# Kernel tuning notes

Hardware: AMD Instinct MI355X
Metric: run time of the kernel (lower is better)

The kernel has to match this reference:

```python
import jax, jax.numpy as jnp
import numpy as np

N = 40000          # nodes
E = 640000         # edges (avg degree 16)
D_MODEL = 128
H = 8              # num_heads
DH = 16            # d_head
DFF = 512
CLAMP = 5.0
EPS = 1e-5


def setup_inputs() -> dict:
    key = jax.random.key(0)
    ks = jax.random.split(key, 10)
    s = 0.08  # weight init scale
    return {
        "feat": jax.random.normal(ks[0], (N, D_MODEL), dtype=jnp.float32),
        "src": jax.random.randint(ks[1], (E,), 0, N, dtype=jnp.int32),
        "dst": jax.random.randint(ks[2], (E,), 0, N, dtype=jnp.int32),
        "Wq": jax.random.normal(ks[3], (H * DH, D_MODEL), dtype=jnp.float32) * s,
        "Wk": jax.random.normal(ks[4], (H * DH, D_MODEL), dtype=jnp.float32) * s,
        "Wv": jax.random.normal(ks[5], (H * DH, D_MODEL), dtype=jnp.float32) * s,
        "Wo": jax.random.normal(ks[6], (D_MODEL, H * DH), dtype=jnp.float32) * s,
        "ln1_g": jnp.ones((D_MODEL,), jnp.float32),
        "ln1_b": jnp.zeros((D_MODEL,), jnp.float32),
        "W1": jax.random.normal(ks[7], (DFF, D_MODEL), dtype=jnp.float32) * s,
        "b1": jnp.zeros((DFF,), jnp.float32),
        "W2": jax.random.normal(ks[8], (D_MODEL, DFF), dtype=jnp.float32) * s,
        "b2": jnp.zeros((D_MODEL,), jnp.float32),
        "ln2_g": jnp.ones((D_MODEL,), jnp.float32),
        "ln2_b": jnp.zeros((D_MODEL,), jnp.float32),
    }


def _layer_norm(x, g, b):
    mu = jnp.mean(x, axis=-1, keepdims=True)
    var = jnp.mean(jnp.square(x - mu), axis=-1, keepdims=True)
    return (x - mu) * jax.lax.rsqrt(var + EPS) * g + b


def reference(feat, src, dst, Wq, Wk, Wv, Wo, ln1_g, ln1_b, W1, b1, W2, b2, ln2_g, ln2_b):
    n = feat.shape[0]
    # Node-level projections (equivalent to DGL's per-edge Linear on gathered feats)
    q = (feat @ Wq.T).reshape(n, H, DH)
    k = (feat @ Wk.T).reshape(n, H, DH)
    v = (feat @ Wv.T).reshape(n, H, DH)

    # Per-edge multi-head attention logits: q[dst] . k[src] / sqrt(d_head), clamped
    u = jnp.sum(q[dst] * k[src], axis=-1) / np.sqrt(DH)   # [E, H]
    u = jnp.clip(u, -CLAMP, CLAMP)

    # Ragged edge-softmax over incoming edges of each dst node
    m = jax.ops.segment_max(u, dst, num_segments=n)        # [N, H]
    e = jnp.exp(u - m[dst])                                # [E, H]
    denom = jax.ops.segment_sum(e, dst, num_segments=n)    # [N, H]
    a = e / denom[dst]                                     # [E, H]

    # Weighted V scatter-reduce back to dst nodes
    av = (a[:, :, None] * v[src]).reshape(-1, H * DH)      # [E, H*DH]
    sum_av = jax.ops.segment_sum(av, dst, num_segments=n)  # [N, H*DH]
    uh = sum_av @ Wo.T                                     # [N, d_model]

    h1 = _layer_norm(feat + uh, ln1_g, ln1_b)
    ffn = jax.nn.relu(h1 @ W1.T + b1) @ W2.T + b2
    return _layer_norm(h1 + ffn, ln2_g, ln2_b)
```

## Files before the change

### kernel.cpp

```cpp
#include <hip/hip_runtime.h>

#define DM 128
#define DFF 512
#define CLAMP_V 5.0f
#define LN_EPS 1e-5f

typedef __attribute__((ext_vector_type(8))) short bf16x8;
typedef __attribute__((ext_vector_type(4))) float f32x4;
typedef __attribute__((ext_vector_type(2))) float f32x2;

__device__ __forceinline__ float b2f(ushort u) {
  union { uint u; float f; } x; x.u = ((uint)u) << 16; return x.f;
}
__device__ __forceinline__ ushort f2b(float f) {
  union { float f; uint u; } x; x.f = f;
  uint r = x.u + 0x7FFFu + ((x.u >> 16) & 1u);
  return (ushort)(r >> 16);
}
__device__ __forceinline__ f32x2 upk2(uint w) {
  union { uint u; float f; } a, b;
  a.u = w << 16; b.u = w & 0xFFFF0000u;
  f32x2 r; r[0] = a.f; r[1] = b.f; return r;
}

__global__ void k_prep(const float* __restrict__ feat,
                       const float* __restrict__ wq, const float* __restrict__ wk,
                       const float* __restrict__ wv, const float* __restrict__ wo,
                       const float* __restrict__ w1, const float* __restrict__ w2,
                       ushort* __restrict__ feat_bf, ushort* __restrict__ wbf,
                       const int* __restrict__ dst, int* __restrict__ deg,
                       int nf4, int castBlocks, int E) {
  if ((int)blockIdx.x >= castBlocks) {
    int e = ((int)blockIdx.x - castBlocks) * 256 + threadIdx.x;
    if (e < E) atomicAdd(&deg[dst[e]], 1);
    return;
  }
  int i = blockIdx.x * 256 + threadIdx.x;
  if (i < nf4) {
    float4 v = *reinterpret_cast<const float4*>(feat + i * 4);
    ushort4 o; o.x = f2b(v.x); o.y = f2b(v.y); o.z = f2b(v.z); o.w = f2b(v.w);
    *reinterpret_cast<ushort4*>(feat_bf + i * 4) = o;
    return;
  }
  int i4 = (i - nf4) * 4;
  if (i4 >= 196608) return;
  const float* s; int o;
  if      (i4 < 16384)  { s = wq; o = i4; }
  else if (i4 < 32768)  { s = wk; o = i4 - 16384; }
  else if (i4 < 49152)  { s = wv; o = i4 - 32768; }
  else if (i4 < 65536)  { s = wo; o = i4 - 49152; }
  else if (i4 < 131072) { s = w1; o = i4 - 65536; }
  else                  { s = w2; o = i4 - 131072; }
  float4 v = *reinterpret_cast<const float4*>(s + o);
  ushort4 u; u.x = f2b(v.x); u.y = f2b(v.y); u.z = f2b(v.z); u.w = f2b(v.w);
  *reinterpret_cast<ushort4*>(wbf + i4) = u;
}

#define SC_EPB 1024

__global__ __launch_bounds__(256) void k_scan(const int* __restrict__ deg,
                                              int* __restrict__ off,
                                              int* __restrict__ cur,
                                              int n, int E) {
  __shared__ int sh[256];
  __shared__ int wsum[4];
  const int t = threadIdx.x;
  const int bstart = blockIdx.x * SC_EPB;

  int gs = 0;
  for (int base = t * 4; base < bstart; base += SC_EPB) {
    int4 v = *reinterpret_cast<const int4*>(deg + base);
    gs += v.x + v.y + v.z + v.w;
  }
  #pragma unroll
  for (int m = 1; m < 64; m <<= 1) gs += __shfl_xor(gs, m);
  if ((t & 63) == 0) wsum[t >> 6] = gs;
  __syncthreads();
  int gadd = wsum[0] + wsum[1] + wsum[2] + wsum[3];
  __syncthreads();

  int base = bstart + t * 4;
  int4 v = {0, 0, 0, 0};
  if (base + 3 < n) {
    v = *reinterpret_cast<const int4*>(deg + base);
  } else {
    if (base     < n) v.x = deg[base];
    if (base + 1 < n) v.y = deg[base + 1];
    if (base + 2 < n) v.z = deg[base + 2];
    if (base + 3 < n) v.w = deg[base + 3];
  }
  int s = v.x + v.y + v.z + v.w;
  sh[t] = s;
  __syncthreads();
  #pragma unroll
  for (int d = 1; d < 256; d <<= 1) {
    int x = 0;
    if (t >= d) x = sh[t - d];
    __syncthreads();
    sh[t] += x;
    __syncthreads();
  }
  int ex = sh[t] - s + gadd;
  if (base + 3 < n) {
    int4 o; o.x = ex; o.y = ex + v.x; o.z = ex + v.x + v.y; o.w = ex + v.x + v.y + v.z;
    *reinterpret_cast<int4*>(off + base) = o;
    int4 z = {0, 0, 0, 0};
    *reinterpret_cast<int4*>(cur + base) = z;
  } else {
    if (base     < n) { off[base]     = ex;                    cur[base]     = 0; }
    if (base + 1 < n) { off[base + 1] = ex + v.x;              cur[base + 1] = 0; }
    if (base + 2 < n) { off[base + 2] = ex + v.x + v.y;        cur[base + 2] = 0; }
    if (base + 3 < n) { off[base + 3] = ex + v.x + v.y + v.z;  cur[base + 3] = 0; }
  }
  if (blockIdx.x == 0 && t == 0) off[n] = E;
}

__global__ __launch_bounds__(512, 2) void k_sqkv(
    const ushort* __restrict__ A, const ushort* __restrict__ W,
    ushort* __restrict__ Cb, ushort* __restrict__ Cb2, int M,
    const int* __restrict__ src, const int* __restrict__ dst,
    const int* __restrict__ off, int* __restrict__ cur,
    int* __restrict__ csr, int E, int qkvB)
{
  __shared__ ushort As[128 * 128];
  __shared__ ushort Bs[128 * 128];

  if ((int)blockIdx.x >= qkvB) {
    int e = ((int)blockIdx.x - qkvB) * 512 + threadIdx.x;
    if (e < E) {
      int d = dst[e];
      int p = off[d] + atomicAdd(&cur[d], 1);
      csr[p] = src[e];
    }
    return;
  }

  const int tid = threadIdx.x;
  const int wv = tid >> 6, ln = tid & 63;
  const int bnb = blockIdx.x % 3;
  const int mbase = (blockIdx.x / 3) * 128;
  const int wrow = (wv >> 2) * 64, wcol = (wv & 3) * 32;
  const int o_base = tid * 16;

  #pragma unroll
  for (int is = 0; is < 4; ++is) {
    int o = is * 8192 + o_base;
    int row = o >> 8;
    int c = ((o >> 4) & 15) ^ (row & 15);
    int gr = min(mbase + row, M - 1);
    const ushort* sA = A + (size_t)gr * 128 + c * 8;
    __builtin_amdgcn_global_load_lds(
        (const __attribute__((address_space(1))) void*)sA,
        (__attribute__((address_space(3))) void*)((char*)As + is * 8192 + wv * 1024),
        16, 0, 0);
    const ushort* sB = W + (size_t)(bnb * 128 + row) * 128 + c * 8;
    __builtin_amdgcn_global_load_lds(
        (const __attribute__((address_space(1))) void*)sB,
        (__attribute__((address_space(3))) void*)((char*)Bs + is * 8192 + wv * 1024),
        16, 0, 0);
  }
  __syncthreads();

  f32x4 acc[4][2] = {};
  const char* AsB = (const char*)As;
  const char* BsB = (const char*)Bs;
  #pragma unroll
  for (int kk = 0; kk < 4; ++kk) {
    bf16x8 af[4], bfr[2];
    #pragma unroll
    for (int m = 0; m < 4; ++m) {
      int r = wrow + m * 16 + (ln & 15);
      int c = kk * 4 + (ln >> 4);
      af[m] = *reinterpret_cast<const bf16x8*>(AsB + r * 256 + ((c ^ (r & 15)) << 4));
    }
    #pragma unroll
    for (int n = 0; n < 2; ++n) {
      int r = wcol + n * 16 + (ln & 15);
      int c = kk * 4 + (ln >> 4);
      bfr[n] = *reinterpret_cast<const bf16x8*>(BsB + r * 256 + ((c ^ (r & 15)) << 4));
    }
    #pragma unroll
    for (int m = 0; m < 4; ++m)
      #pragma unroll
      for (int n = 0; n < 2; ++n)
        acc[m][n] = __builtin_amdgcn_mfma_f32_16x16x32_bf16(af[m], bfr[n], acc[m][n], 0, 0, 0);
  }

  #pragma unroll
  for (int m = 0; m < 4; ++m) {
    int gr0 = mbase + wrow + m * 16 + (ln >> 4) * 4;
    #pragma unroll
    for (int n = 0; n < 2; ++n) {
      int gcl = wcol + n * 16 + (ln & 15);
      #pragma unroll
      for (int r = 0; r < 4; ++r) {
        int gr = gr0 + r;
        if (gr >= M) continue;
        float v = acc[m][n][r];
        if (bnb == 0) Cb[(size_t)gr * 128 + gcl] = f2b(v);
        else          Cb2[(size_t)gr * 256 + (bnb - 1) * 128 + gcl] = f2b(v);
      }
    }
  }
}

template<int FLAGS, bool OUTF, bool OUTB>
__global__ __launch_bounds__(512, 2) void k_mmT(
    const ushort* __restrict__ A, const ushort* __restrict__ W,
    const float* __restrict__ res,
    const float* __restrict__ lng, const float* __restrict__ lnbv,
    float* __restrict__ Cf, ushort* __restrict__ Cb, int M)
{
  __shared__ ushort As[128 * 128];
  __shared__ ushort Bs[128 * 128];
  __shared__ float lnred[1024];

  const int tid = threadIdx.x;
  const int wv = tid >> 6, ln = tid & 63;
  const int mbase = blockIdx.y * 128;
  const int wrow = (wv >> 2) * 64, wcol = (wv & 3) * 32;
  const int o_base = tid * 16;

  #pragma unroll
  for (int is = 0; is < 4; ++is) {
    int o = is * 8192 + o_base;
    int row = o >> 8;
    int c = ((o >> 4) & 15) ^ (row & 15);
    int gr = min(mbase + row, M - 1);
    const ushort* sA = A + (size_t)gr * 128 + c * 8;
    __builtin_amdgcn_global_load_lds(
        (const __attribute__((address_space(1))) void*)sA,
        (__attribute__((address_space(3))) void*)((char*)As + is * 8192 + wv * 1024),
        16, 0, 0);
    const ushort* sB = W + (size_t)row * 128 + c * 8;
    __builtin_amdgcn_global_load_lds(
        (const __attribute__((address_space(1))) void*)sB,
        (__attribute__((address_space(3))) void*)((char*)Bs + is * 8192 + wv * 1024),
        16, 0, 0);
  }
  __syncthreads();

  f32x4 acc[4][2] = {};
  const char* AsB = (const char*)As;
  const char* BsB = (const char*)Bs;
  #pragma unroll
  for (int kk = 0; kk < 4; ++kk) {
    bf16x8 af[4], bfr[2];
    #pragma unroll
    for (int m = 0; m < 4; ++m) {
      int r = wrow + m * 16 + (ln & 15);
      int c = kk * 4 + (ln >> 4);
      af[m] = *reinterpret_cast<const bf16x8*>(AsB + r * 256 + ((c ^ (r & 15)) << 4));
    }
    #pragma unroll
    for (int n = 0; n < 2; ++n) {
      int r = wcol + n * 16 + (ln & 15);
      int c = kk * 4 + (ln >> 4);
      bfr[n] = *reinterpret_cast<const bf16x8*>(BsB + r * 256 + ((c ^ (r & 15)) << 4));
    }
    #pragma unroll
    for (int m = 0; m < 4; ++m)
      #pragma unroll
      for (int n = 0; n < 2; ++n)
        acc[m][n] = __builtin_amdgcn_mfma_f32_16x16x32_bf16(af[m], bfr[n], acc[m][n], 0, 0, 0);
  }

  #pragma unroll
  for (int m = 0; m < 4; ++m)
    #pragma unroll
    for (int n = 0; n < 2; ++n) {
      int gc = wcol + n * 16 + (ln & 15);
      #pragma unroll
      for (int r = 0; r < 4; ++r) {
        int gr = mbase + wrow + m * 16 + (ln >> 4) * 4 + r;
        float v = acc[m][n][r];
        if (FLAGS & 4) v += res[(size_t)min(gr, M - 1) * 128 + gc];
        acc[m][n][r] = v;
      }
    }
  #pragma unroll
  for (int m = 0; m < 4; ++m)
    #pragma unroll
    for (int r = 0; r < 4; ++r) {
      float sm = acc[m][0][r] + acc[m][1][r];
      float sq = acc[m][0][r] * acc[m][0][r] + acc[m][1][r] * acc[m][1][r];
      #pragma unroll
      for (int msk = 1; msk <= 8; msk <<= 1) {
        sm += __shfl_xor(sm, msk);
        sq += __shfl_xor(sq, msk);
      }
      if ((ln & 15) == 0) {
        int row = wrow + m * 16 + (ln >> 4) * 4 + r;
        lnred[row * 8 + (wv & 3) * 2]     = sm;
        lnred[row * 8 + (wv & 3) * 2 + 1] = sq;
      }
    }
  __syncthreads();
  #pragma unroll
  for (int m = 0; m < 4; ++m)
    #pragma unroll
    for (int r = 0; r < 4; ++r) {
      int row = wrow + m * 16 + (ln >> 4) * 4 + r;
      int gr = mbase + row;
      float sm = lnred[row * 8] + lnred[row * 8 + 2] + lnred[row * 8 + 4] + lnred[row * 8 + 6];
      float sq = lnred[row * 8 + 1] + lnred[row * 8 + 3] + lnred[row * 8 + 5] + lnred[row * 8 + 7];
      float mu = sm * (1.f / 128.f);
      float var = fmaxf(sq * (1.f / 128.f) - mu * mu, 0.f);
      float rstd = rsqrtf(var + LN_EPS);
      if (gr < M) {
        #pragma unroll
        for (int n = 0; n < 2; ++n) {
          int gc = wcol + n * 16 + (ln & 15);
          float y = (acc[m][n][r] - mu) * rstd * lng[gc] + lnbv[gc];
          if (OUTF) Cf[(size_t)gr * 128 + gc] = y;
          if (OUTB) Cb[(size_t)gr * 128 + gc] = f2b(y);
        }
      }
    }
}

__global__ __launch_bounds__(512, 2) void k_ffn(
    const ushort* __restrict__ h1b,
    const ushort* __restrict__ w1, const float* __restrict__ b1,
    const ushort* __restrict__ w2, const float* __restrict__ b2,
    const float* __restrict__ lng, const float* __restrict__ lnbv,
    float* __restrict__ outp, int M)
{
  __shared__ ushort mid[64 * 512];
  __shared__ ushort wbuf[2][128 * 128];

  const int tid = threadIdx.x;
  const int wv = tid >> 6, ln = tid & 63;
  const int lr = ln & 15, hi = ln >> 4;
  const int mbase = blockIdx.x * 64;
  const int gc = wv * 16 + lr;

  auto STG128 = [&](const ushort* srcBase, int srcLd, int colOff, char* dstLds) {
    #pragma unroll
    for (int is = 0; is < 4; ++is) {
      int o = is * 8192 + tid * 16;
      int r = o >> 8;
      int c = ((o >> 4) & 15) ^ (r & 15);
      const ushort* s = srcBase + (size_t)r * srcLd + colOff + c * 8;
      __builtin_amdgcn_global_load_lds(
          (const __attribute__((address_space(1))) void*)s,
          (__attribute__((address_space(3))) void*)(dstLds + is * 8192 + wv * 1024),
          16, 0, 0);
    }
  };

  #pragma unroll
  for (int is = 0; is < 2; ++is) {
    int o = is * 8192 + tid * 16;
    int r = o >> 8;
    int c = ((o >> 4) & 15) ^ (r & 15);
    int gr = min(mbase + r, M - 1);
    const ushort* s = h1b + (size_t)gr * 128 + c * 8;
    __builtin_amdgcn_global_load_lds(
        (const __attribute__((address_space(1))) void*)s,
        (__attribute__((address_space(3))) void*)((char*)mid + is * 8192 + wv * 1024),
        16, 0, 0);
  }
  STG128(w1, 128, 0, (char*)wbuf[0]);
  __syncthreads();

  f32x4 p1[4][4] = {};
  const char* hB = (const char*)mid;
  #pragma unroll
  for (int g = 0; g < 4; ++g) {
    const int buf = g & 1;
    if (g < 3) STG128(w1 + (size_t)(g + 1) * 128 * 128, 128, 0, (char*)wbuf[buf ^ 1]);
    else       STG128(w2, 512, 0, (char*)wbuf[buf ^ 1]);
    const char* wB = (const char*)wbuf[buf];
    #pragma unroll
    for (int kk = 0; kk < 4; ++kk) {
      int c = kk * 4 + hi;
      int wr = wv * 16 + lr;
      bf16x8 aW = *reinterpret_cast<const bf16x8*>(wB + wr * 256 + ((c ^ (wr & 15)) << 4));
      bf16x8 bH[4];
      #pragma unroll
      for (int hj = 0; hj < 4; ++hj) {
        int r = hj * 16 + lr;
        bH[hj] = *reinterpret_cast<const bf16x8*>(hB + r * 256 + ((c ^ (r & 15)) << 4));
      }
      #pragma unroll
      for (int hj = 0; hj < 4; ++hj)
        p1[g][hj] = __builtin_amdgcn_mfma_f32_16x16x32_bf16(aW, bH[hj], p1[g][hj], 0, 0, 0);
    }
    __syncthreads();
  }

  float h1res[4][4];
  {
    int chunk = gc >> 3;
    int sub = (gc & 7) * 2;
    #pragma unroll
    for (int m = 0; m < 4; ++m)
      #pragma unroll
      for (int r = 0; r < 4; ++r) {
        int row = m * 16 + hi * 4 + r;
        h1res[m][r] = b2f(*reinterpret_cast<const ushort*>(
            (const char*)mid + row * 256 + ((chunk ^ (row & 15)) << 4) + sub));
      }
  }
  __syncthreads();

  #pragma unroll
  for (int g = 0; g < 4; ++g) {
    int mc0 = g * 128 + wv * 16 + hi * 4;
    float4 bv = *reinterpret_cast<const float4*>(b1 + mc0);
    int chunk = mc0 >> 3;
    int sub = (mc0 & 7) * 2;
    #pragma unroll
    for (int hj = 0; hj < 4; ++hj) {
      int orow = hj * 16 + lr;
      ushort4 pk;
      pk.x = f2b(fmaxf(p1[g][hj][0] + bv.x, 0.f));
      pk.y = f2b(fmaxf(p1[g][hj][1] + bv.y, 0.f));
      pk.z = f2b(fmaxf(p1[g][hj][2] + bv.z, 0.f));
      pk.w = f2b(fmaxf(p1[g][hj][3] + bv.w, 0.f));
      char* dstp = (char*)mid + orow * 1024 + (((chunk & 63) ^ (orow & 15)) << 4) + sub;
      *reinterpret_cast<ushort4*>(dstp) = pk;
    }
  }
  __syncthreads();

  f32x4 p2[4] = {};
  #pragma unroll
  for (int g2 = 0; g2 < 4; ++g2) {
    const int buf = g2 & 1;
    if (g2 < 3) STG128(w2, 512, (g2 + 1) * 128, (char*)wbuf[buf ^ 1]);
    const char* wB = (const char*)wbuf[buf];
    #pragma unroll
    for (int kk = 0; kk < 4; ++kk) {
      int wr = wv * 16 + lr;
      int cw = kk * 4 + hi;
      bf16x8 bW = *reinterpret_cast<const bf16x8*>(wB + wr * 256 + ((cw ^ (wr & 15)) << 4));
      int cm = g2 * 16 + kk * 4 + hi;
      bf16x8 aM[4];
      #pragma unroll
      for (int m = 0; m < 4; ++m) {
        int r = m * 16 + lr;
        aM[m] = *reinterpret_cast<const bf16x8*>((const char*)mid + r * 1024 + (((cm & 63) ^ (r & 15)) << 4));
      }
      #pragma unroll
      for (int m = 0; m < 4; ++m)
        p2[m] = __builtin_amdgcn_mfma_f32_16x16x32_bf16(aM[m], bW, p2[m], 0, 0, 0);
    }
    __syncthreads();
  }

  float* lnred = reinterpret_cast<float*>(&wbuf[0][0]);
  {
    float bsv = b2[gc];
    #pragma unroll
    for (int m = 0; m < 4; ++m)
      #pragma unroll
      for (int r = 0; r < 4; ++r)
        p2[m][r] += bsv + h1res[m][r];
  }
  #pragma unroll
  for (int m = 0; m < 4; ++m)
    #pragma unroll
    for (int r = 0; r < 4; ++r) {
      float sm = p2[m][r];
      float sq = p2[m][r] * p2[m][r];
      #pragma unroll
      for (int msk = 1; msk <= 8; msk <<= 1) {
        sm += __shfl_xor(sm, msk);
        sq += __shfl_xor(sq, msk);
      }
      if (lr == 0) {
        int row = m * 16 + hi * 4 + r;
        lnred[row * 16 + wv * 2]     = sm;
        lnred[row * 16 + wv * 2 + 1] = sq;
      }
    }
  __syncthreads();
  {
    float g2v = lng[gc], bb2 = lnbv[gc];
    #pragma unroll
    for (int m = 0; m < 4; ++m)
      #pragma unroll
      for (int r = 0; r < 4; ++r) {
        int row = m * 16 + hi * 4 + r;
        int gr = mbase + row;
        float sm = 0.f, sq = 0.f;
        #pragma unroll
        for (int w = 0; w < 8; ++w) {
          sm += lnred[row * 16 + w * 2];
          sq += lnred[row * 16 + w * 2 + 1];
        }
        float mu = sm * (1.f / 128.f);
        float var = fmaxf(sq * (1.f / 128.f) - mu * mu, 0.f);
        float rstd = rsqrtf(var + LN_EPS);
        if (gr < M)
          outp[(size_t)gr * 128 + gc] = (p2[m][r] - mu) * rstd * g2v + bb2;
      }
  }
}

__global__ __launch_bounds__(256) void k_attn(
    const ushort* __restrict__ q, const ushort* __restrict__ kv,
    const int* __restrict__ off, const int* __restrict__ csr,
    ushort* __restrict__ sav, int n)
{
  int node = blockIdx.x * 4 + (threadIdx.x >> 6);
  int lane = threadIdx.x & 63;
  if (node >= n) return;
  const int g = lane >> 3, sl = lane & 7;

  const ushort* qr = q + (size_t)node * 128 + sl * 16;
  uint4 qw0 = *reinterpret_cast<const uint4*>(qr);
  uint4 qw1 = *reinterpret_cast<const uint4*>(qr + 8);
  f32x2 qv[8];
  qv[0] = upk2(qw0.x); qv[1] = upk2(qw0.y); qv[2] = upk2(qw0.z); qv[3] = upk2(qw0.w);
  qv[4] = upk2(qw1.x); qv[5] = upk2(qw1.y); qv[6] = upk2(qw1.z); qv[7] = upk2(qw1.w);

  int b = off[node], e = off[node + 1];
  float s = 0.f;
  f32x2 a2[8] = {};
  int nIt = (e - b + 7) >> 3;
  int idx = b + g;
  int sn = (b < e) ? csr[min(idx, e - 1)] : 0;

  for (int i = 0; i < nIt; ++i) {
    bool act = idx < e;
    const ushort* kr = kv + (size_t)sn * 256 + sl * 16;
    uint4 kw0 = *reinterpret_cast<const uint4*>(kr);
    uint4 kw1 = *reinterpret_cast<const uint4*>(kr + 8);
    uint4 vw0 = *reinterpret_cast<const uint4*>(kr + 128);
    uint4 vw1 = *reinterpret_cast<const uint4*>(kr + 136);
    idx += 8;
    if (i + 1 < nIt) sn = csr[min(idx, e - 1)];

    f32x2 acc = qv[0] * upk2(kw0.x);
    acc += qv[1] * upk2(kw0.y);
    acc += qv[2] * upk2(kw0.z);
    acc += qv[3] * upk2(kw0.w);
    acc += qv[4] * upk2(kw1.x);
    acc += qv[5] * upk2(kw1.y);
    acc += qv[6] * upk2(kw1.z);
    acc += qv[7] * upk2(kw1.w);
    float p = acc[0] + acc[1];
    float u = fminf(fmaxf(p * 0.25f, -CLAMP_V), CLAMP_V);
    float w = __expf(u - CLAMP_V);
    w = act ? w : 0.f;
    s += w;
    f32x2 w2; w2[0] = w; w2[1] = w;
    a2[0] += w2 * upk2(vw0.x);
    a2[1] += w2 * upk2(vw0.y);
    a2[2] += w2 * upk2(vw0.z);
    a2[3] += w2 * upk2(vw0.w);
    a2[4] += w2 * upk2(vw1.x);
    a2[5] += w2 * upk2(vw1.y);
    a2[6] += w2 * upk2(vw1.z);
    a2[7] += w2 * upk2(vw1.w);
  }

  #pragma unroll
  for (int msk = 8; msk <= 32; msk <<= 1) {
    s += __shfl_xor(s, msk);
    #pragma unroll
    for (int j = 0; j < 8; ++j) {
      a2[j][0] += __shfl_xor(a2[j][0], msk);
      a2[j][1] += __shfl_xor(a2[j][1], msk);
    }
  }

  float inv = (s > 0.f) ? 1.f / s : 0.f;
  if (g == 0) {
    uint w[8];
    #pragma unroll
    for (int j = 0; j < 8; ++j)
      w[j] = (uint)f2b(a2[j][0] * inv) | ((uint)f2b(a2[j][1] * inv) << 16);
    ushort* outp = sav + (size_t)node * 128 + sl * 16;
    uint4 o0 = {w[0], w[1], w[2], w[3]};
    uint4 o1 = {w[4], w[5], w[6], w[7]};
    *reinterpret_cast<uint4*>(outp) = o0;
    *reinterpret_cast<uint4*>(outp + 8) = o1;
  }
}

extern "C" void kernel_launch(void* const* d_in, const int* in_sizes, int n_in,
                              void* d_out, int out_size, void* d_ws, size_t ws_size,
                              hipStream_t stream)
{
  const float* feat = (const float*)d_in[0];
  const int*   src  = (const int*)d_in[1];
  const int*   dst  = (const int*)d_in[2];
  const float* Wq   = (const float*)d_in[3];
  const float* Wk   = (const float*)d_in[4];
  const float* Wv   = (const float*)d_in[5];
  const float* Wo   = (const float*)d_in[6];
  const float* ln1g = (const float*)d_in[7];
  const float* ln1b = (const float*)d_in[8];
  const float* W1   = (const float*)d_in[9];
  const float* b1   = (const float*)d_in[10];
  const float* W2   = (const float*)d_in[11];
  const float* b2   = (const float*)d_in[12];
  const float* ln2g = (const float*)d_in[13];
  const float* ln2b = (const float*)d_in[14];
  float* out = (float*)d_out;

  const int N = in_sizes[0] / DM;
  const int E = in_sizes[1];
  const size_t NB = (size_t)N;

  char* wsb = (char*)d_ws;
  ushort* q_bf    = (ushort*)wsb;
  ushort* kv_bf   = (ushort*)(wsb + NB * 256);
  ushort* sav_bf  = (ushort*)(wsb + NB * 768);
  ushort* h1b     = (ushort*)(wsb + NB * 1536);
  ushort* feat_bf = (ushort*)(wsb + NB * 1792);
  ushort* wbf     = (ushort*)(wsb + NB * 2048);
  ushort* wqkv_bf = wbf;
  ushort* wo_bf   = wbf + 49152;
  ushort* w1_bf   = wbf + 65536;
  ushort* w2_bf   = wbf + 131072;
  int* ib  = (int*)(wbf + 196608);
  int* deg = ib;
  int* cur = ib + N;
  int* off = ib + 2 * N;
  int* csr = ib + 3 * N + 1;

  hipMemsetAsync(deg, 0, (size_t)N * sizeof(int), stream);

  int nf4 = N * DM / 4;
  int castBlocks = (nf4 + 49152 + 255) / 256;
  int cntBlocks = (E + 255) / 256;
  k_prep<<<castBlocks + cntBlocks, 256, 0, stream>>>(
      feat, Wq, Wk, Wv, Wo, W1, W2, feat_bf, wbf, dst, deg, nf4, castBlocks, E);

  int nbk = (N + SC_EPB - 1) / SC_EPB;
  k_scan<<<nbk, 256, 0, stream>>>(deg, off, cur, N, E);

  const int nT = (N + 127) / 128;
  int qkvB = 3 * nT;
  int scB = (E + 511) / 512;
  k_sqkv<<<qkvB + scB, 512, 0, stream>>>(
      feat_bf, wqkv_bf, q_bf, kv_bf, N, src, dst, off, cur, csr, E, qkvB);

  int nb4 = (N + 3) / 4;
  k_attn<<<nb4, 256, 0, stream>>>(q_bf, kv_bf, off, csr, sav_bf, N);

  k_mmT<4 | 8, false, true><<<dim3(1, nT), 512, 0, stream>>>(
      sav_bf, wo_bf, feat, ln1g, ln1b, nullptr, h1b, N);

  const int nF = (N + 63) / 64;
  k_ffn<<<nF, 512, 0, stream>>>(
      h1b, w1_bf, b1, w2_bf, b2, ln2g, ln2b, out, N);
}
```

Before: 192.2 us.

## Split scatter from QKV GEMM and shrink FFN tile to 32 rows for occupancy

The CSR scatter moves out of the fused QKV GEMM launch into its own kernel, and the QKV GEMM now uses a 2D grid. The FFN kernel processes 32 rows per block instead of 64, streams weights in 64-column halves so LDS use drops, and raises launch bounds to 4 blocks per SM for more occupancy. This adds a kernel launch and more weight reloads per row in exchange for more concurrent blocks and less register and LDS pressure.

New measurement: 190.6 us. About the same (-0.8%).

```diff
diff --git a/kernel.cpp b/kernel.cpp
--- a/kernel.cpp
+++ b/kernel.cpp
@@ -115,30 +115,28 @@
   if (blockIdx.x == 0 && t == 0) off[n] = E;
 }
 
-__global__ __launch_bounds__(512, 2) void k_sqkv(
+__global__ void k_scatter(const int* __restrict__ src, const int* __restrict__ dst,
+                          const int* __restrict__ off, int* __restrict__ cur,
+                          int* __restrict__ csr, int E) {
+  int e = blockIdx.x * blockDim.x + threadIdx.x;
+  if (e < E) {
+    int d = dst[e];
+    int p = off[d] + atomicAdd(&cur[d], 1);
+    csr[p] = src[e];
+  }
+}
+
+__global__ __launch_bounds__(512, 2) void k_qkv(
     const ushort* __restrict__ A, const ushort* __restrict__ W,
-    ushort* __restrict__ Cb, ushort* __restrict__ Cb2, int M,
-    const int* __restrict__ src, const int* __restrict__ dst,
-    const int* __restrict__ off, int* __restrict__ cur,
-    int* __restrict__ csr, int E, int qkvB)
+    ushort* __restrict__ Cb, ushort* __restrict__ Cb2, int M)
 {
   __shared__ ushort As[128 * 128];
   __shared__ ushort Bs[128 * 128];
 
-  if ((int)blockIdx.x >= qkvB) {
-    int e = ((int)blockIdx.x - qkvB) * 512 + threadIdx.x;
-    if (e < E) {
-      int d = dst[e];
-      int p = off[d] + atomicAdd(&cur[d], 1);
-      csr[p] = src[e];
-    }
-    return;
-  }
-
   const int tid = threadIdx.x;
   const int wv = tid >> 6, ln = tid & 63;
-  const int bnb = blockIdx.x % 3;
-  const int mbase = (blockIdx.x / 3) * 128;
+  const int bnb = blockIdx.x;
+  const int mbase = blockIdx.y * 128;
   const int wrow = (wv >> 2) * 64, wcol = (wv & 3) * 32;
   const int o_base = tid * 16;
 
@@ -204,12 +202,11 @@
   }
 }
 
-template<int FLAGS, bool OUTF, bool OUTB>
 __global__ __launch_bounds__(512, 2) void k_mmT(
     const ushort* __restrict__ A, const ushort* __restrict__ W,
     const float* __restrict__ res,
     const float* __restrict__ lng, const float* __restrict__ lnbv,
-    float* __restrict__ Cf, ushort* __restrict__ Cb, int M)
+    ushort* __restrict__ Cb, int M)
 {
   __shared__ ushort As[128 * 128];
   __shared__ ushort Bs[128 * 128];
@@ -273,9 +270,7 @@
       #pragma unroll
       for (int r = 0; r < 4; ++r) {
         int gr = mbase + wrow + m * 16 + (ln >> 4) * 4 + r;
-        float v = acc[m][n][r];
-        if (FLAGS & 4) v += res[(size_t)min(gr, M - 1) * 128 + gc];
-        acc[m][n][r] = v;
+        acc[m][n][r] += res[(size_t)min(gr, M - 1) * 128 + gc];
       }
     }
   #pragma unroll
@@ -312,35 +307,35 @@
         for (int n = 0; n < 2; ++n) {
           int gc = wcol + n * 16 + (ln & 15);
           float y = (acc[m][n][r] - mu) * rstd * lng[gc] + lnbv[gc];
-          if (OUTF) Cf[(size_t)gr * 128 + gc] = y;
-          if (OUTB) Cb[(size_t)gr * 128 + gc] = f2b(y);
+          Cb[(size_t)gr * 128 + gc] = f2b(y);
         }
       }
     }
 }
 
-__global__ __launch_bounds__(512, 2) void k_ffn(
+__global__ __launch_bounds__(512, 4) void k_ffn(
     const ushort* __restrict__ h1b,
     const ushort* __restrict__ w1, const float* __restrict__ b1,
     const ushort* __restrict__ w2, const float* __restrict__ b2,
     const float* __restrict__ lng, const float* __restrict__ lnbv,
     float* __restrict__ outp, int M)
 {
-  __shared__ ushort mid[64 * 512];
-  __shared__ ushort wbuf[2][128 * 128];
+  __shared__ ushort mid[32 * 512];
+  __shared__ ushort wbuf[2][128 * 64];
+  __shared__ float lnred[32 * 16];
 
   const int tid = threadIdx.x;
   const int wv = tid >> 6, ln = tid & 63;
   const int lr = ln & 15, hi = ln >> 4;
-  const int mbase = blockIdx.x * 64;
+  const int mbase = blockIdx.x * 32;
   const int gc = wv * 16 + lr;
 
-  auto STG128 = [&](const ushort* srcBase, int srcLd, int colOff, char* dstLds) {
-    #pragma unroll
-    for (int is = 0; is < 4; ++is) {
+  auto STG64 = [&](const ushort* srcBase, int srcLd, int colOff, char* dstLds) {
+    #pragma unroll
+    for (int is = 0; is < 2; ++is) {
       int o = is * 8192 + tid * 16;
-      int r = o >> 8;
-      int c = ((o >> 4) & 15) ^ (r & 15);
+      int r = o >> 7;
+      int c = ((o >> 4) & 7) ^ (r & 7);
       const ushort* s = srcBase + (size_t)r * srcLd + colOff + c * 8;
       __builtin_amdgcn_global_load_lds(
           (const __attribute__((address_space(1))) void*)s,
@@ -349,53 +344,60 @@
     }
   };
 
-  #pragma unroll
-  for (int is = 0; is < 2; ++is) {
-    int o = is * 8192 + tid * 16;
+  {
+    int o = tid * 16;
     int r = o >> 8;
     int c = ((o >> 4) & 15) ^ (r & 15);
     int gr = min(mbase + r, M - 1);
     const ushort* s = h1b + (size_t)gr * 128 + c * 8;
     __builtin_amdgcn_global_load_lds(
         (const __attribute__((address_space(1))) void*)s,
-        (__attribute__((address_space(3))) void*)((char*)mid + is * 8192 + wv * 1024),
+        (__attribute__((address_space(3))) void*)((char*)mid + wv * 1024),
         16, 0, 0);
   }
-  STG128(w1, 128, 0, (char*)wbuf[0]);
-  __syncthreads();
-
-  f32x4 p1[4][4] = {};
+  STG64(w1, 128, 0, (char*)wbuf[0]);
+  __syncthreads();
+
+  f32x4 p1[4][2] = {};
   const char* hB = (const char*)mid;
   #pragma unroll
   for (int g = 0; g < 4; ++g) {
-    const int buf = g & 1;
-    if (g < 3) STG128(w1 + (size_t)(g + 1) * 128 * 128, 128, 0, (char*)wbuf[buf ^ 1]);
-    else       STG128(w2, 512, 0, (char*)wbuf[buf ^ 1]);
-    const char* wB = (const char*)wbuf[buf];
-    #pragma unroll
-    for (int kk = 0; kk < 4; ++kk) {
-      int c = kk * 4 + hi;
-      int wr = wv * 16 + lr;
-      bf16x8 aW = *reinterpret_cast<const bf16x8*>(wB + wr * 256 + ((c ^ (wr & 15)) << 4));
-      bf16x8 bH[4];
-      #pragma unroll
-      for (int hj = 0; hj < 4; ++hj) {
-        int r = hj * 16 + lr;
-        bH[hj] = *reinterpret_cast<const bf16x8*>(hB + r * 256 + ((c ^ (r & 15)) << 4));
-      }
-      #pragma unroll
-      for (int hj = 0; hj < 4; ++hj)
-        p1[g][hj] = __builtin_amdgcn_mfma_f32_16x16x32_bf16(aW, bH[hj], p1[g][hj], 0, 0, 0);
-    }
-    __syncthreads();
-  }
-
-  float h1res[4][4];
+    #pragma unroll
+    for (int kh = 0; kh < 2; ++kh) {
+      const int step = g * 2 + kh;
+      if (step < 7) {
+        int ns = step + 1;
+        STG64(w1 + (size_t)(ns >> 1) * 128 * 128, 128, (ns & 1) * 64, (char*)wbuf[ns & 1]);
+      } else {
+        STG64(w2, 512, 0, (char*)wbuf[0]);
+      }
+      const char* wB = (const char*)wbuf[step & 1];
+      #pragma unroll
+      for (int kk = 0; kk < 2; ++kk) {
+        int ct = kk * 4 + hi;
+        int cg = kh * 8 + ct;
+        int wr = wv * 16 + lr;
+        bf16x8 aW = *reinterpret_cast<const bf16x8*>(wB + wr * 128 + ((ct ^ (wr & 7)) << 4));
+        bf16x8 bH[2];
+        #pragma unroll
+        for (int hj = 0; hj < 2; ++hj) {
+          int r = hj * 16 + lr;
+          bH[hj] = *reinterpret_cast<const bf16x8*>(hB + r * 256 + ((cg ^ (r & 15)) << 4));
+        }
+        #pragma unroll
+        for (int hj = 0; hj < 2; ++hj)
+          p1[g][hj] = __builtin_amdgcn_mfma_f32_16x16x32_bf16(aW, bH[hj], p1[g][hj], 0, 0, 0);
+      }
+      __syncthreads();
+    }
+  }
+
+  float h1res[2][4];
   {
     int chunk = gc >> 3;
     int sub = (gc & 7) * 2;
     #pragma unroll
-    for (int m = 0; m < 4; ++m)
+    for (int m = 0; m < 2; ++m)
       #pragma unroll
       for (int r = 0; r < 4; ++r) {
         int row = m * 16 + hi * 4 + r;
@@ -412,7 +414,7 @@
     int chunk = mc0 >> 3;
     int sub = (mc0 & 7) * 2;
     #pragma unroll
-    for (int hj = 0; hj < 4; ++hj) {
+    for (int hj = 0; hj < 2; ++hj) {
       int orow = hj * 16 + lr;
       ushort4 pk;
       pk.x = f2b(fmaxf(p1[g][hj][0] + bv.x, 0.f));
@@ -425,42 +427,40 @@
   }
   __syncthreads();
 
-  f32x4 p2[4] = {};
-  #pragma unroll
-  for (int g2 = 0; g2 < 4; ++g2) {
-    const int buf = g2 & 1;
-    if (g2 < 3) STG128(w2, 512, (g2 + 1) * 128, (char*)wbuf[buf ^ 1]);
-    const char* wB = (const char*)wbuf[buf];
-    #pragma unroll
-    for (int kk = 0; kk < 4; ++kk) {
+  f32x4 p2[2] = {};
+  #pragma unroll
+  for (int kt = 0; kt < 8; ++kt) {
+    if (kt < 7) STG64(w2, 512, (kt + 1) * 64, (char*)wbuf[(kt + 1) & 1]);
+    const char* wB = (const char*)wbuf[kt & 1];
+    #pragma unroll
+    for (int kk = 0; kk < 2; ++kk) {
+      int ct = kk * 4 + hi;
+      int cm = kt * 8 + ct;
       int wr = wv * 16 + lr;
-      int cw = kk * 4 + hi;
-      bf16x8 bW = *reinterpret_cast<const bf16x8*>(wB + wr * 256 + ((cw ^ (wr & 15)) << 4));
-      int cm = g2 * 16 + kk * 4 + hi;
-      bf16x8 aM[4];
-      #pragma unroll
-      for (int m = 0; m < 4; ++m) {
+      bf16x8 bW = *reinterpret_cast<const bf16x8*>(wB + wr * 128 + ((ct ^ (wr & 7)) << 4));
+      bf16x8 aM[2];
+      #pragma unroll
+      for (int m = 0; m < 2; ++m) {
         int r = m * 16 + lr;
         aM[m] = *reinterpret_cast<const bf16x8*>((const char*)mid + r * 1024 + (((cm & 63) ^ (r & 15)) << 4));
       }
       #pragma unroll
-      for (int m = 0; m < 4; ++m)
+      for (int m = 0; m < 2; ++m)
         p2[m] = __builtin_amdgcn_mfma_f32_16x16x32_bf16(aM[m], bW, p2[m], 0, 0, 0);
     }
     __syncthreads();
   }
 
-  float* lnred = reinterpret_cast<float*>(&wbuf[0][0]);
   {
     float bsv = b2[gc];
     #pragma unroll
-    for (int m = 0; m < 4; ++m)
+    for (int m = 0; m < 2; ++m)
       #pragma unroll
       for (int r = 0; r < 4; ++r)
         p2[m][r] += bsv + h1res[m][r];
   }
   #pragma unroll
-  for (int m = 0; m < 4; ++m)
+  for (int m = 0; m < 2; ++m)
     #pragma unroll
     for (int r = 0; r < 4; ++r) {
       float sm = p2[m][r];
@@ -480,7 +480,7 @@
   {
     float g2v = lng[gc], bb2 = lnbv[gc];
     #pragma unroll
-    for (int m = 0; m < 4; ++m)
+    for (int m = 0; m < 2; ++m)
       #pragma unroll
       for (int r = 0; r < 4; ++r) {
         int row = m * 16 + hi * 4 + r;
@@ -547,15 +547,15 @@
     float w = __expf(u - CLAMP_V);
     w = act ? w : 0.f;
     s += w;
-    f32x2 w2; w2[0] = w; w2[1] = w;
-    a2[0] += w2 * upk2(vw0.x);
-    a2[1] += w2 * upk2(vw0.y);
-    a2[2] += w2 * upk2(vw0.z);
-    a2[3] += w2 * upk2(vw0.w);
-    a2[4] += w2 * upk2(vw1.x);
-    a2[5] += w2 * upk2(vw1.y);
-    a2[6] += w2 * upk2(vw1.z);
-    a2[7] += w2 * upk2(vw1.w);
+    f32x2 w2v; w2v[0] = w; w2v[1] = w;
+    a2[0] += w2v * upk2(vw0.x);
+    a2[1] += w2v * upk2(vw0.y);
+    a2[2] += w2v * upk2(vw0.z);
+    a2[3] += w2v * upk2(vw0.w);
+    a2[4] += w2v * upk2(vw1.x);
+    a2[5] += w2v * upk2(vw1.y);
+    a2[6] += w2v * upk2(vw1.z);
+    a2[7] += w2v * upk2(vw1.w);
   }
 
   #pragma unroll
@@ -634,20 +634,17 @@
 
   int nbk = (N + SC_EPB - 1) / SC_EPB;
   k_scan<<<nbk, 256, 0, stream>>>(deg, off, cur, N, E);
+  k_scatter<<<cntBlocks, 256, 0, stream>>>(src, dst, off, cur, csr, E);
 
   const int nT = (N + 127) / 128;
-  int qkvB = 3 * nT;
-  int scB = (E + 511) / 512;
-  k_sqkv<<<qkvB + scB, 512, 0, stream>>>(
-      feat_bf, wqkv_bf, q_bf, kv_bf, N, src, dst, off, cur, csr, E, qkvB);
+  k_qkv<<<dim3(3, nT), 512, 0, stream>>>(feat_bf, wqkv_bf, q_bf, kv_bf, N);
 
   int nb4 = (N + 3) / 4;
   k_attn<<<nb4, 256, 0, stream>>>(q_bf, kv_bf, off, csr, sav_bf, N);
 
-  k_mmT<4 | 8, false, true><<<dim3(1, nT), 512, 0, stream>>>(
-      sav_bf, wo_bf, feat, ln1g, ln1b, nullptr, h1b, N);
-
-  const int nF = (N + 63) / 64;
+  k_mmT<<<dim3(1, nT), 512, 0, stream>>>(sav_bf, wo_bf, feat, ln1g, ln1b, h1b, N);
+
+  const int nF = (N + 31) / 32;
   k_ffn<<<nF, 512, 0, stream>>>(
       h1b, w1_bf, b1, w2_bf, b2, ln2g, ln2b, out, N);
 }
```
